# Optimization experiments

Measured on AMD Instinct MI355X. Metric: run time of the kernel, lower is better.

## Reference

```python
import jax, jax.numpy as jnp
import numpy as np

P, NL, NQ, L, P2L, P2Q, D = 50000, 2000, 6000, 8, 128, 64, 32
MAX_MODELS, NPOL, MAXQ, ITERS = 7, 4, 3, 8
ZS = {'traffic': (1385.4059, 859.8119), 'packets': (1.4015, 0.8933), 'eq_lambda': (1350.9712, 858.3162), 'avg_pkts_lambda': (0.9117, 0.9724), 'exp_max_factor': (6.6636, 4.7151), 'pkts_lambda_on': (0.9116, 1.6513), 'avg_t_off': (1.6649, 2.3564), 'avg_t_on': (1.6649, 2.3564), 'ar_a': (0.0, 1.0), 'sigma': (0.0, 1.0), 'capacity': (27611.0918, 20090.6211), 'queue_size': (30259.1055, 21410.0957)}


def _glorot(k, fin, fout):
    lim = float(np.sqrt(6.0 / (fin + fout)))
    return jax.random.uniform(k, (fin, fout), jnp.float32, -lim, lim)


def setup_inputs():
    keys = iter(jax.random.split(jax.random.key(0), 80))
    nk = lambda: next(keys)
    u = lambda shape, lo=0.0, hi=1.0: jax.random.uniform(nk(), shape, jnp.float32, lo, hi)
    inp = {}
    inp['traffic'] = u((P, 1), 1.0, 3000.0)
    inp['packets'] = u((P, 1), 0.5, 3.0)
    inp['eq_lambda'] = u((P, 1), 1.0, 3000.0)
    inp['avg_pkts_lambda'] = u((P, 1))
    inp['exp_max_factor'] = u((P, 1), 1.0, 12.0)
    inp['pkts_lambda_on'] = u((P, 1))
    inp['avg_t_off'] = u((P, 1), 0.1, 4.0)
    inp['avg_t_on'] = u((P, 1), 0.1, 4.0)
    inp['ar_a'] = jax.random.normal(nk(), (P, 1), jnp.float32)
    inp['sigma'] = jax.random.normal(nk(), (P, 1), jnp.float32)
    inp['capacity'] = u((NL, 1), 8000.0, 60000.0)
    inp['queue_size'] = u((NQ, 1), 1000.0, 64000.0)
    inp['weight'] = u((NQ, 1))
    length = jax.random.randint(nk(), (P,), 1, L + 1)
    inp['length'] = length
    inp['model'] = jax.random.randint(nk(), (P,), 0, MAX_MODELS)
    inp['policy'] = jax.random.randint(nk(), (NL,), 0, NPOL)
    inp['priority'] = jax.random.randint(nk(), (NQ,), 0, MAXQ)
    inp['queue_to_path'] = jax.random.randint(nk(), (P, L), 0, NQ)
    inp['link_to_path'] = jax.random.randint(nk(), (P, L), 0, NL)
    p2l_path = jax.random.randint(nk(), (NL, P2L), 0, P)
    inp['path_to_link'] = jnp.stack([p2l_path, jnp.zeros_like(p2l_path)], -1)
    inp['p2l_deg'] = jax.random.randint(nk(), (NL,), 1, P2L + 1)
    pq_path = jax.random.randint(nk(), (NQ, P2Q), 0, P)
    pq_pos = 1 + jax.random.randint(nk(), (NQ, P2Q), 0, L) % length[pq_path]
    inp['path_to_queue'] = jnp.stack([pq_path, pq_pos], -1)
    inp['p2q_deg'] = jax.random.randint(nk(), (NQ,), 1, P2Q + 1)
    inp['queue_to_link'] = jnp.arange(NL * MAXQ).reshape(NL, MAXQ)
    def dense(fin, fout):
        return _glorot(nk(), fin, fout), jnp.zeros((fout,), jnp.float32)
    inp['pe_w1'], inp['pe_b1'] = dense(10 + MAX_MODELS, D)
    inp['pe_w2'], inp['pe_b2'] = dense(D, D)
    inp['le_w1'], inp['le_b1'] = dense(NPOL + 1, D)
    inp['le_w2'], inp['le_b2'] = dense(D, D)
    inp['qe_w1'], inp['qe_b1'] = dense(MAXQ + 2, D)
    inp['qe_w2'], inp['qe_b2'] = dense(D, D)
    inp['prW'] = _glorot(nk(), 2 * D, D); inp['prU'] = _glorot(nk(), D, D); inp['prB'] = jnp.zeros((D,), jnp.float32)
    inp['qrW'] = _glorot(nk(), D, D); inp['qrU'] = _glorot(nk(), D, D); inp['qrB'] = jnp.zeros((D,), jnp.float32)
    inp['lrW'] = _glorot(nk(), D, D); inp['lrU'] = _glorot(nk(), D, D); inp['lrB'] = jnp.zeros((D,), jnp.float32)
    inp['ro_w1'], inp['ro_b1'] = dense(D, D // 2)
    inp['ro_w2'], inp['ro_b2'] = dense(D // 2, D // 2)
    inp['ro_w3'], inp['ro_b3'] = dense(D // 2, 1)
    return inp


def _mlp2(x, w1, b1, w2, b2):
    return jax.nn.relu(jax.nn.relu(x @ w1 + b1) @ w2 + b2)


def _forward(traffic, packets, eq_lambda, avg_pkts_lambda, exp_max_factor, pkts_lambda_on,
             avg_t_off, avg_t_on, ar_a, sigma, capacity, queue_size, weight,
             pe_w1, pe_b1, pe_w2, pe_b2, le_w1, le_b1, le_w2, le_b2, qe_w1, qe_b1, qe_w2, qe_b2,
             prW, prU, prB, qrW, qrU, qrB, lrW, lrU, lrB,
             ro_w1, ro_b1, ro_w2, ro_b2, ro_w3, ro_b3,
             length, model, policy, priority, queue_to_path, link_to_path,
             path_to_link, path_to_queue, queue_to_link, p2l_deg, p2q_deg):
    dt = traffic.dtype
    nz = lambda x, k: (x - ZS[k][0]) / ZS[k][1]
    # link load: masked ragged sum of traffic of paths crossing each link
    p2l_mask = (jnp.arange(P2L) < p2l_deg[:, None]).astype(dt)                # [NL, P2L]
    path_gather_traffic = traffic[path_to_link[:, :, 0], 0]                   # [NL, P2L]
    load = (path_gather_traffic * p2l_mask).sum(1, keepdims=True) / capacity  # [NL, 1]
    pkt_size = traffic / packets                                              # [P, 1]
    path_features = jnp.concatenate([
        nz(traffic, 'traffic'), nz(packets, 'packets'),
        jax.nn.one_hot(model, MAX_MODELS, dtype=dt),
        nz(eq_lambda, 'eq_lambda'), nz(avg_pkts_lambda, 'avg_pkts_lambda'),
        nz(exp_max_factor, 'exp_max_factor'), nz(pkts_lambda_on, 'pkts_lambda_on'),
        nz(avg_t_off, 'avg_t_off'), nz(avg_t_on, 'avg_t_on'),
        nz(ar_a, 'ar_a'), nz(sigma, 'sigma')], axis=1)                         # [P, 17]
    path_state = _mlp2(path_features, pe_w1, pe_b1, pe_w2, pe_b2)             # [P, D]
    link_state = _mlp2(jnp.concatenate([load, jax.nn.one_hot(policy, NPOL, dtype=dt)], 1),
                       le_w1, le_b1, le_w2, le_b2)                             # [NL, D]
    queue_state = _mlp2(jnp.concatenate([nz(queue_size, 'queue_size'),
                                         jax.nn.one_hot(priority, MAXQ, dtype=dt), weight], 1),
                        qe_w1, qe_b1, qe_w2, qe_b2)                            # [NQ, D]
    hop_mask = (jnp.arange(L) < length[:, None]).astype(dt)                    # [P, L]
    p2q_mask = (jnp.arange(P2Q) < p2q_deg[:, None]).astype(dt)                 # [NQ, P2Q]

    def path_step(h, xs):
        x_t, m_t = xs
        h_new = jnp.tanh(x_t @ prW + h @ prU + prB)
        h = m_t[:, None] * h_new + (1.0 - m_t[:, None]) * h  # ragged: freeze past length
        return h, h

    pss = None
    for _ in range(ITERS):
        qg = queue_state[queue_to_path]                                        # [P, L, D]
        lg = link_state[link_to_path]                                          # [P, L, D]
        xin = jnp.concatenate([qg, lg], -1)                                    # [P, L, 2D]
        prev = path_state
        path_state, seq = jax.lax.scan(path_step, path_state,
                                       (jnp.swapaxes(xin, 0, 1), hop_mask.T))
        pss = jnp.concatenate([prev[:, None], jnp.swapaxes(seq, 0, 1)], 1)     # [P, L+1, D]
        pg = pss[path_to_queue[:, :, 0], path_to_queue[:, :, 1]]               # [NQ, P2Q, D]
        path_sum = (pg * p2q_mask[:, :, None]).sum(1)                          # [NQ, D]
        queue_state = jnp.tanh(path_sum @ qrW + queue_state @ qrU + qrB)
        qgl = queue_state[queue_to_link]                                       # [NL, 3, D]
        h = link_state
        for t in range(MAXQ):  # fixed tiny sequence of 3 queues per link
            h = jnp.tanh(qgl[:, t] @ lrW + h @ lrU + lrB)
        link_state = h
    cap_g = capacity[link_to_path, 0]                                          # [P, L]
    occ = jax.nn.relu(pss[:, 1:] @ ro_w1 + ro_b1)
    occ = jax.nn.relu(occ @ ro_w2 + ro_b2)
    occ = (occ @ ro_w3 + ro_b3)[:, :, 0]                                       # [P, L]
    queue_delay = ((occ / cap_g) * hop_mask).sum(1, keepdims=True)             # [P, 1]
    trans_delay = pkt_size * ((1.0 / cap_g) * hop_mask).sum(1, keepdims=True)  # [P, 1]
    return queue_delay + trans_delay


def reference(traffic, packets, eq_lambda, avg_pkts_lambda, exp_max_factor, pkts_lambda_on,
              avg_t_off, avg_t_on, ar_a, sigma, capacity, queue_size, weight,
              pe_w1, pe_b1, pe_w2, pe_b2, le_w1, le_b1, le_w2, le_b2, qe_w1, qe_b1, qe_w2, qe_b2,
              prW, prU, prB, qrW, qrU, qrB, lrW, lrU, lrB,
              ro_w1, ro_b1, ro_w2, ro_b2, ro_w3, ro_b3,
              length, model, policy, priority, queue_to_path, link_to_path,
              path_to_link, path_to_queue, queue_to_link, p2l_deg, p2q_deg):
    return _forward(traffic, packets, eq_lambda, avg_pkts_lambda, exp_max_factor, pkts_lambda_on,
                    avg_t_off, avg_t_on, ar_a, sigma, capacity, queue_size, weight,
                    pe_w1, pe_b1, pe_w2, pe_b2, le_w1, le_b1, le_w2, le_b2, qe_w1, qe_b1, qe_w2, qe_b2,
                    prW, prU, prB, qrW, qrU, qrB, lrW, lrU, lrB,
                    ro_w1, ro_b1, ro_w2, ro_b2, ro_w3, ro_b3,
                    length, model, policy, priority, queue_to_path, link_to_path,
                    path_to_link, path_to_queue, queue_to_link, p2l_deg, p2q_deg)
```

## Files before the change

kernel.cpp:

```cpp
#include <hip/hip_runtime.h>
#include <hip/hip_bf16.h>

#define P_ 50000
#define NL_ 2000
#define NQ_ 6000
#define L_ 8
#define P2L_ 128
#define P2Q_ 64
#define D_ 32
#define ITERS_ 8
#define RA_ 1563
#define RC_ 1500

typedef __hip_bfloat16 bf16;
typedef unsigned short u16;
typedef unsigned int u32;

__device__ __forceinline__ float bfb2f(u16 u) {
    union { u32 i; float f; } c; c.i = ((u32)u) << 16; return c.f;
}
__device__ __forceinline__ u16 f2bfb(float f) {
    union { bf16 h; u16 u; } c; c.h = __float2bfloat16(f); return c.u;
}
__device__ __forceinline__ u32 pk2(float a, float b) {
    return (u32)f2bfb(a) | ((u32)f2bfb(b) << 16);
}

__device__ __forceinline__ float tanh_fast(float x) {
    return 1.f - 2.f / (__expf(2.f * x) + 1.f);
}
__device__ __forceinline__ float4 tanh4(float4 a) {
    return make_float4(tanh_fast(a.x), tanh_fast(a.y), tanh_fast(a.z), tanh_fast(a.w));
}

__device__ __forceinline__ void hr_rebuild(float* hr, float4 own) {
    hr[0] = own.x; hr[1] = own.y; hr[2] = own.z; hr[3] = own.w;
#pragma unroll
    for (int c = 0; c < 4; c++)  hr[4 + c]  = __shfl_xor(hr[c], 1, 64);
#pragma unroll
    for (int c = 0; c < 8; c++)  hr[8 + c]  = __shfl_xor(hr[c], 2, 64);
#pragma unroll
    for (int c = 0; c < 16; c++) hr[16 + c] = __shfl_xor(hr[c], 4, 64);
}

__device__ __forceinline__ float4 matvec32o(const float* hr, const float* base,
                                            const int* offs, float4 acc) {
#pragma unroll
    for (int s = 0; s < 8; s++) {
        const float* u0 = base + offs[s];
#pragma unroll
        for (int c = 0; c < 4; c++) {
            const float4 u = *(const float4*)(u0 + 32 * c);
            const float hk = hr[4 * s + c];
            acc.x += hk * u.x; acc.y += hk * u.y;
            acc.z += hk * u.z; acc.w += hk * u.w;
        }
    }
    return acc;
}

__device__ bool detect_f32(const void* p, int n) {
    const u16* u = (const u16*)p;
    int m = n < 64 ? n : 64;
    bool bad = false;
    for (int k = 0; k < m; k++) {
        float v = bfb2f(u[k]);
        float av = fabsf(v);
        bool sane = (v == v) && (av <= 1e6f) && (av == 0.0f || av >= 1e-8f);
        bad |= !sane;
    }
    return bad;
}


struct CvtArgs { const void* p[40]; };

__global__ __launch_bounds__(256) void k_convert(CvtArgs a, float* __restrict__ dst,
                                                 int* __restrict__ counters) {
    static constexpr int N[40] = {
        50000,50000,50000,50000,50000,50000,50000,50000,50000,50000,
        2000,6000,6000,
        544,32,1024,32, 160,32,1024,32, 160,32,1024,32,
        2048,1024,32, 1024,1024,32, 1024,1024,32,
        512,16,256,16,16,1};
    if (blockIdx.x == 0 && threadIdx.x < 16) counters[threadIdx.x] = 0;
    int b = blockIdx.x, t = 0, off = 0;
    for (;;) {
        int nb = (N[t] + 255) >> 8;
        if (b < nb) break;
        b -= nb; off += N[t]; ++t;
    }
    const void* src = a.p[t];
    const int n = N[t];
    const bool isf = detect_f32(src, n);
    if (t == 0 && b == 0 && threadIdx.x == 0) counters[16] = isf ? 1 : 0;
    const int i = b * 256 + threadIdx.x;
    if (i < n)
        dst[off + i] = isf ? ((const float*)src)[i] : bfb2f(((const u16*)src)[i]);
}


__global__ __launch_bounds__(256) void k_hist(const int* __restrict__ length,
                                              int* __restrict__ hist) {
    __shared__ int hc[8];
    const int tid = threadIdx.x;
    if (tid < 8) hc[tid] = 0;
    __syncthreads();
    int p = blockIdx.x * 256 + tid;
    if (p < P_) atomicAdd(&hc[length[p] - 1], 1);
    __syncthreads();
    if (tid < 8 && hc[tid] > 0) atomicAdd(&hist[tid], hc[tid]);
}

__global__ __launch_bounds__(256) void k_scatter(const int* __restrict__ length,
                                                 const int* __restrict__ hist,
                                                 int* __restrict__ cursor,
                                                 int* __restrict__ perm,
                                                 int* __restrict__ inv) {
    __shared__ int cnt[8];
    __shared__ int base[8];
    const int tid = threadIdx.x;
    if (tid < 8) cnt[tid] = 0;
    __syncthreads();
    const int p = blockIdx.x * 256 + tid;
    int b = 0, r = 0;
    if (p < P_) { b = length[p] - 1; r = atomicAdd(&cnt[b], 1); }
    __syncthreads();
    if (tid < 8) {
        int pre = 0;
#pragma unroll
        for (int k = 0; k < 8; k++) pre += (k > tid) ? hist[k] : 0;
        base[tid] = pre + (cnt[tid] > 0 ? atomicAdd(&cursor[tid], cnt[tid]) : 0);
    }
    __syncthreads();
    if (p < P_) { const int pos = base[b] + r; perm[pos] = p; inv[p] = pos; }
}


__global__ __launch_bounds__(256) void k_remap(
    const int* __restrict__ perm, const int* __restrict__ inv,
    const int* __restrict__ q2p, const int* __restrict__ l2p,
    const int* __restrict__ length, const int* __restrict__ p2q,
    int* __restrict__ q2ps, int* __restrict__ l2ps, int* __restrict__ lens,
    int* __restrict__ p2qs)
{
    const int blk = blockIdx.x;
    if (blk < RA_) {
        const int idx = blk * 256 + threadIdx.x;
        if (idx >= P_ * 8) return;
        const int j = idx >> 3, t = idx & 7;
        const int p = perm[j];
        q2ps[idx] = q2p[p * 8 + t];
        l2ps[idx] = l2p[p * 8 + t];
        if (t == 0) lens[j] = length[p];
    } else {
        const int e = (blk - RA_) * 256 + threadIdx.x;
        if (e >= NQ_ * P2Q_) return;
        const int2 pr = ((const int2*)p2q)[e];
        ((int2*)p2qs)[e] = make_int2(inv[pr.x], pr.y);
    }
}


__global__ __launch_bounds__(256) void k_path_embed(
    const float* __restrict__ traffic, const float* __restrict__ packets,
    const float* __restrict__ eq_lambda, const float* __restrict__ avg_pkts_lambda,
    const float* __restrict__ exp_max_factor, const float* __restrict__ pkts_lambda_on,
    const float* __restrict__ avg_t_off, const float* __restrict__ avg_t_on,
    const float* __restrict__ ar_a, const float* __restrict__ sigma,
    const int* __restrict__ model, const int* __restrict__ inv,
    const float* __restrict__ w1, const float* __restrict__ b1,
    const float* __restrict__ w2, const float* __restrict__ b2,
    float* __restrict__ sps)
{
    __shared__ float s_w1[544], s_w2[1024], s_b1[32], s_b2[32];
    const int tid = threadIdx.x;
    for (int idx = tid; idx < 544; idx += 256)  s_w1[idx] = w1[idx];
    for (int idx = tid; idx < 1024; idx += 256) s_w2[idx] = w2[idx];
    if (tid < 32) { s_b1[tid] = b1[tid]; s_b2[tid] = b2[tid]; }
    __syncthreads();

    int p = blockIdx.x * 256 + tid;
    if (p >= P_) return;
    float f[10];
    f[0] = (traffic[p]        - 1385.4059f) * (1.f / 859.8119f);
    f[1] = (packets[p]        - 1.4015f)    * (1.f / 0.8933f);
    f[2] = (eq_lambda[p]      - 1350.9712f) * (1.f / 858.3162f);
    f[3] = (avg_pkts_lambda[p]- 0.9117f)    * (1.f / 0.9724f);
    f[4] = (exp_max_factor[p] - 6.6636f)    * (1.f / 4.7151f);
    f[5] = (pkts_lambda_on[p] - 0.9116f)    * (1.f / 1.6513f);
    f[6] = (avg_t_off[p]      - 1.6649f)    * (1.f / 2.3564f);
    f[7] = (avg_t_on[p]       - 1.6649f)    * (1.f / 2.3564f);
    f[8] = ar_a[p];
    f[9] = sigma[p];
    const int mrow = 2 + model[p];
    float h1[32];
#pragma unroll
    for (int d = 0; d < 32; d++) {
        float a = s_b1[d] + s_w1[mrow * 32 + d];
        a += f[0] * s_w1[0 * 32 + d];
        a += f[1] * s_w1[1 * 32 + d];
#pragma unroll
        for (int j = 0; j < 8; j++) a += f[2 + j] * s_w1[(9 + j) * 32 + d];
        h1[d] = fmaxf(a, 0.f);
    }
    float* dst = sps + (size_t)inv[p] * 32;
#pragma unroll
    for (int d = 0; d < 32; d++) {
        float a = s_b2[d];
#pragma unroll
        for (int k = 0; k < 32; k++) a += h1[k] * s_w2[k * 32 + d];
        dst[d] = fmaxf(a, 0.f);
    }
}


__global__ __launch_bounds__(256) void k_queue_embed(
    const float* __restrict__ queue_size, const float* __restrict__ weight,
    const int* __restrict__ priority,
    const float* __restrict__ w1, const float* __restrict__ b1,
    const float* __restrict__ w2, const float* __restrict__ b2,
    const float* __restrict__ prW, const float* __restrict__ prB,
    float* __restrict__ queue_state, float* __restrict__ zq)
{
    __shared__ float s_w1[160], s_w2[1024], s_pw[1024], s_b1[32], s_b2[32], s_pb[32];
    const int tid = threadIdx.x;
    if (tid < 160) s_w1[tid] = w1[tid];
    for (int idx = tid; idx < 1024; idx += 256) {
        s_w2[idx] = w2[idx];
        s_pw[idx] = prW[idx];
    }
    if (tid < 32) { s_b1[tid] = b1[tid]; s_b2[tid] = b2[tid]; s_pb[tid] = prB[tid]; }
    __syncthreads();

    int q = blockIdx.x * 256 + tid;
    if (q >= NQ_) return;
    float f0 = (queue_size[q] - 30259.1055f) * (1.f / 21410.0957f);
    float f4 = weight[q];
    int prow = 1 + priority[q];
    float h1[32];
#pragma unroll
    for (int d = 0; d < 32; d++) {
        float a = s_b1[d] + s_w1[prow * 32 + d]
                + f0 * s_w1[0 * 32 + d] + f4 * s_w1[4 * 32 + d];
        h1[d] = fmaxf(a, 0.f);
    }
    float h2[32];
#pragma unroll
    for (int d = 0; d < 32; d++) {
        float a = s_b2[d];
#pragma unroll
        for (int k = 0; k < 32; k++) a += h1[k] * s_w2[k * 32 + d];
        h2[d] = fmaxf(a, 0.f);
        queue_state[q * 32 + d] = h2[d];
    }
#pragma unroll
    for (int d = 0; d < 32; d++) {
        float a = s_pb[d];
#pragma unroll
        for (int k = 0; k < 32; k++) a += h2[k] * s_pw[k * 32 + d];
        zq[q * 32 + d] = a;
    }
}


__global__ __launch_bounds__(256) void k_link_embed(
    const float* __restrict__ traffic, const float* __restrict__ capacity,
    const int* __restrict__ policy,
    const int* __restrict__ p2l, const int* __restrict__ p2l_deg,
    const float* __restrict__ w1, const float* __restrict__ b1,
    const float* __restrict__ w2, const float* __restrict__ b2,
    const float* __restrict__ prWl,
    float* __restrict__ link_state, float* __restrict__ zl)
{
    __shared__ float wsh[2272];
    __shared__ float h1s[4][32];
    __shared__ float h2s[4][32];
    const int tid = threadIdx.x;
    if (tid < 160) wsh[tid] = w1[tid];
    if (tid < 32)  wsh[160 + tid] = b1[tid];
    for (int idx = tid; idx < 1024; idx += 256) {
        wsh[192 + idx]  = w2[idx];
        wsh[1248 + idx] = prWl[idx];
    }
    if (tid >= 32 && tid < 64) wsh[1216 + tid - 32] = b2[tid - 32];
    __syncthreads();

    const int w = tid >> 6, lane = tid & 63;
    const int l = blockIdx.x * 4 + w;
    const int deg = p2l_deg[l];
    float s = 0.f;
    if (lane < deg)      s += traffic[p2l[l * 256 + 2 * lane]];
    if (lane + 64 < deg) s += traffic[p2l[l * 256 + 2 * (lane + 64)]];
#pragma unroll
    for (int m = 1; m < 64; m <<= 1) s += __shfl_xor(s, m, 64);
    const float load = s / capacity[l];
    const int prow = 1 + policy[l];
    if (lane < 32) {
        float a = wsh[160 + lane] + wsh[prow * 32 + lane] + load * wsh[lane];
        h1s[w][lane] = fmaxf(a, 0.f);
    }
    __syncthreads();
    if (lane < 32) {
        float a = wsh[1216 + lane];
#pragma unroll
        for (int k = 0; k < 32; k++) a += h1s[w][k] * wsh[192 + k * 32 + lane];
        a = fmaxf(a, 0.f);
        link_state[l * 32 + lane] = a;
        h2s[w][lane] = a;
    }
    __syncthreads();
    if (lane < 32) {
        float a = 0.f;
#pragma unroll
        for (int k = 0; k < 32; k++) a += h2s[w][k] * wsh[1248 + k * 32 + lane];
        zl[l * 32 + lane] = a;
    }
}


__global__ __launch_bounds__(256, 2) void k_path_rnn(
    const int* __restrict__ q2ps, const int* __restrict__ l2ps,
    const int* __restrict__ lens,
    const float* __restrict__ prU,
    const float* __restrict__ zq, const float* __restrict__ zl,
    float* __restrict__ sps, u16* __restrict__ pss)
{
    const int tid = threadIdx.x;
    const int grp = tid >> 3, i = tid & 7;
    const int j = blockIdx.x * 32 + grp;
    if (j >= P_) return;
    const int len = lens[j];

    float4 Ub[32];
#pragma unroll
    for (int s = 0; s < 8; s++) {
        const float* rb = prU + ((i ^ s) * 128 + 4 * i);
#pragma unroll
        for (int c = 0; c < 4; c++)
            Ub[4 * s + c] = *(const float4*)(rb + 32 * c);
    }

    const int4 qi0 = *(const int4*)(q2ps + (size_t)j * 8);
    const int4 qi1 = *(const int4*)(q2ps + (size_t)j * 8 + 4);
    const int4 li0 = *(const int4*)(l2ps + (size_t)j * 8);
    const int4 li1 = *(const int4*)(l2ps + (size_t)j * 8 + 4);
    const int qidx[8] = {qi0.x, qi0.y, qi0.z, qi0.w, qi1.x, qi1.y, qi1.z, qi1.w};
    const int lidx[8] = {li0.x, li0.y, li0.z, li0.w, li1.x, li1.y, li1.z, li1.w};

    float4 own = *(const float4*)(sps + (size_t)j * 32 + 4 * i);
    float hr[32];
    hr_rebuild(hr, own);

    float4 z;
    {
        const float4 a = *(const float4*)(zq + (size_t)qidx[0] * 32 + 4 * i);
        const float4 b = *(const float4*)(zl + (size_t)lidx[0] * 32 + 4 * i);
        z = make_float4(a.x + b.x, a.y + b.y, a.z + b.z, a.w + b.w);
    }

#pragma unroll
    for (int t = 0; t < 8; t++) {
        if (t >= len) break;
        float4 acc = z;
        if (t + 1 < len) {
            const float4 a = *(const float4*)(zq + (size_t)qidx[t + 1] * 32 + 4 * i);
            const float4 b = *(const float4*)(zl + (size_t)lidx[t + 1] * 32 + 4 * i);
            z = make_float4(a.x + b.x, a.y + b.y, a.z + b.z, a.w + b.w);
        }
#pragma unroll
        for (int k = 0; k < 32; k++) {
            const float hk = hr[k];
            acc.x += hk * Ub[k].x; acc.y += hk * Ub[k].y;
            acc.z += hk * Ub[k].z; acc.w += hk * Ub[k].w;
        }
        own = tanh4(acc);
        uint2 w2;
        w2.x = pk2(own.x, own.y);
        w2.y = pk2(own.z, own.w);
        *(uint2*)(pss + (size_t)j * 256 + t * 32 + 4 * i) = w2;
        if (t + 1 < len) hr_rebuild(hr, own);
    }
    *(float4*)(sps + (size_t)j * 32 + 4 * i) = own;
}


__global__ __launch_bounds__(256, 2) void k_rnn_last(
    const int* __restrict__ q2ps, const int* __restrict__ l2ps,
    const int* __restrict__ lens, const int* __restrict__ perm,
    const float* __restrict__ prU,
    const float* __restrict__ zq, const float* __restrict__ zl,
    const float* __restrict__ sps,
    const float* __restrict__ capacity,
    const float* __restrict__ traffic, const float* __restrict__ packets,
    const float* __restrict__ w1, const float* __restrict__ b1,
    const float* __restrict__ w2, const float* __restrict__ b2,
    const float* __restrict__ w3, const float* __restrict__ b3,
    const int* __restrict__ flags, void* __restrict__ out)
{
    __shared__ float wl[817];
    const int tid = threadIdx.x;
    for (int idx = tid; idx < 512; idx += 256) wl[idx] = w1[idx];
    if (tid < 256) wl[528 + tid] = w2[tid];
    if (tid < 16) {
        wl[512 + tid] = b1[tid];
        wl[784 + tid] = b2[tid];
        wl[800 + tid] = w3[tid];
    }
    if (tid == 0) wl[816] = b3[0];
    __syncthreads();

    const int grp = tid >> 3, i = tid & 7;
    const int j = blockIdx.x * 32 + grp;
    if (j >= P_) return;
    const int len = lens[j];

    float4 Ub[32];
#pragma unroll
    for (int s = 0; s < 8; s++) {
        const float* rb = prU + ((i ^ s) * 128 + 4 * i);
#pragma unroll
        for (int c = 0; c < 4; c++)
            Ub[4 * s + c] = *(const float4*)(rb + 32 * c);
    }

    const int4 qi0 = *(const int4*)(q2ps + (size_t)j * 8);
    const int4 qi1 = *(const int4*)(q2ps + (size_t)j * 8 + 4);
    const int4 li0 = *(const int4*)(l2ps + (size_t)j * 8);
    const int4 li1 = *(const int4*)(l2ps + (size_t)j * 8 + 4);
    const int qidx[8] = {qi0.x, qi0.y, qi0.z, qi0.w, qi1.x, qi1.y, qi1.z, qi1.w};
    const int lidx[8] = {li0.x, li0.y, li0.z, li0.w, li1.x, li1.y, li1.z, li1.w};

    float4 own = *(const float4*)(sps + (size_t)j * 32 + 4 * i);
    float hr[32];
    hr_rebuild(hr, own);

    float4 z;
    {
        const float4 a = *(const float4*)(zq + (size_t)qidx[0] * 32 + 4 * i);
        const float4 b = *(const float4*)(zl + (size_t)lidx[0] * 32 + 4 * i);
        z = make_float4(a.x + b.x, a.y + b.y, a.z + b.z, a.w + b.w);
    }

    float qd = 0.f, ts = 0.f;
#pragma unroll
    for (int t = 0; t < 8; t++) {
        if (t >= len) break;
        float4 acc = z;
        if (t + 1 < len) {
            const float4 a = *(const float4*)(zq + (size_t)qidx[t + 1] * 32 + 4 * i);
            const float4 b = *(const float4*)(zl + (size_t)lidx[t + 1] * 32 + 4 * i);
            z = make_float4(a.x + b.x, a.y + b.y, a.z + b.z, a.w + b.w);
        }
#pragma unroll
        for (int k = 0; k < 32; k++) {
            const float hk = hr[k];
            acc.x += hk * Ub[k].x; acc.y += hk * Ub[k].y;
            acc.z += hk * Ub[k].z; acc.w += hk * Ub[k].w;
        }
        own = tanh4(acc);
        hr_rebuild(hr, own);

        float a0 = wl[512 + 2 * i], a1 = wl[512 + 2 * i + 1];
#pragma unroll
        for (int s = 0; s < 8; s++) {
#pragma unroll
            for (int c = 0; c < 4; c++) {
                const int k = 4 * (i ^ s) + c;
                const float2 u = *(const float2*)&wl[k * 16 + 2 * i];
                const float hk = hr[4 * s + c];
                a0 += hk * u.x; a1 += hk * u.y;
            }
        }
        a0 = fmaxf(a0, 0.f); a1 = fmaxf(a1, 0.f);
        float h2r[16];
        h2r[0] = a0; h2r[1] = a1;
#pragma unroll
        for (int c = 0; c < 2; c++) h2r[2 + c] = __shfl_xor(h2r[c], 1, 64);
#pragma unroll
        for (int c = 0; c < 4; c++) h2r[4 + c] = __shfl_xor(h2r[c], 2, 64);
#pragma unroll
        for (int c = 0; c < 8; c++) h2r[8 + c] = __shfl_xor(h2r[c], 4, 64);
        float c0 = wl[784 + 2 * i], c1 = wl[784 + 2 * i + 1];
#pragma unroll
        for (int s = 0; s < 8; s++) {
#pragma unroll
            for (int c = 0; c < 2; c++) {
                const int k = 2 * (i ^ s) + c;
                const float2 u = *(const float2*)&wl[528 + k * 16 + 2 * i];
                const float hk = h2r[2 * s + c];
                c0 += hk * u.x; c1 += hk * u.y;
            }
        }
        c0 = fmaxf(c0, 0.f); c1 = fmaxf(c1, 0.f);
        float pv = c0 * wl[800 + 2 * i] + c1 * wl[800 + 2 * i + 1];
        pv += __shfl_xor(pv, 1, 8);
        pv += __shfl_xor(pv, 2, 8);
        pv += __shfl_xor(pv, 4, 8);
        const float occv = pv + wl[816];
        const float inv = 1.f / capacity[lidx[t]];
        qd += occv * inv;
        ts += inv;
    }
    if (i == 0) {
        const int p = perm[j];
        const float res = qd + (traffic[p] / packets[p]) * ts;
        if (flags[0]) ((float*)out)[p] = res;
        else          ((bf16*)out)[p] = __float2bfloat16(res);
    }
}


__global__ __launch_bounds__(256) void k_queue_update(
    const int* __restrict__ p2qs, const int* __restrict__ p2q_deg,
    const float* __restrict__ qrW, const float* __restrict__ qrU,
    const float* __restrict__ qrB,
    const float* __restrict__ prWq, const float* __restrict__ prB,
    const u16* __restrict__ pss, float* __restrict__ queue_state,
    float* __restrict__ zq)
{
    __shared__ float wl[3 * 1024 + 64];
    const int tid = threadIdx.x;
#pragma unroll
    for (int jj = 0; jj < 4; jj++) {
        wl[tid + 256 * jj]        = qrW[tid + 256 * jj];
        wl[1024 + tid + 256 * jj] = qrU[tid + 256 * jj];
        wl[2048 + tid + 256 * jj] = prWq[tid + 256 * jj];
    }
    if (tid < 32) { wl[3072 + tid] = qrB[tid]; wl[3104 + tid] = prB[tid]; }
    __syncthreads();

    const int w = tid >> 6, lane = tid & 63;
    const int g = lane >> 3, i = lane & 7;
    const int q = blockIdx.x * 4 + w;
    const int deg = p2q_deg[q];

    int offs[8];
#pragma unroll
    for (int s = 0; s < 8; s++) offs[s] = (i ^ s) * 128 + 4 * i;

    float4 ps = {0.f, 0.f, 0.f, 0.f};
    for (int j = g; j < deg; j += 8) {
        const int2 pr = ((const int2*)p2qs)[q * 64 + j];
        int pos = pr.y - 1;
        pos = pos < 0 ? 0 : (pos > 7 ? 7 : pos);
        const ushort4 v = *(const ushort4*)(pss + (size_t)pr.x * 256 + pos * 32 + 4 * i);
        ps.x += bfb2f(v.x); ps.y += bfb2f(v.y);
        ps.z += bfb2f(v.z); ps.w += bfb2f(v.w);
    }
#pragma unroll
    for (int m = 8; m < 64; m <<= 1) {
        ps.x += __shfl_xor(ps.x, m, 64);
        ps.y += __shfl_xor(ps.y, m, 64);
        ps.z += __shfl_xor(ps.z, m, 64);
        ps.w += __shfl_xor(ps.w, m, 64);
    }
    const float4 qs = *(const float4*)(queue_state + (size_t)q * 32 + 4 * i);

    float psr[32]; hr_rebuild(psr, ps);
    float qsr[32]; hr_rebuild(qsr, qs);
    float4 acc = *(const float4*)(wl + 3072 + 4 * i);
    acc = matvec32o(psr, wl, offs, acc);
    acc = matvec32o(qsr, wl + 1024, offs, acc);
    const float4 nh = tanh4(acc);

    float nhr[32]; hr_rebuild(nhr, nh);
    float4 zacc = *(const float4*)(wl + 3104 + 4 * i);
    zacc = matvec32o(nhr, wl + 2048, offs, zacc);

    if (g == 0) {
        *(float4*)(queue_state + (size_t)q * 32 + 4 * i) = nh;
        *(float4*)(zq + (size_t)q * 32 + 4 * i) = zacc;
    }
}


__global__ __launch_bounds__(256) void k_link_update(
    const int* __restrict__ q2l,
    const float* __restrict__ lrW, const float* __restrict__ lrU,
    const float* __restrict__ lrB,
    const float* __restrict__ prWl,
    const float* __restrict__ queue_state, float* __restrict__ link_state,
    float* __restrict__ zl)
{
    __shared__ float wl[3 * 1024 + 32];
    const int tid = threadIdx.x;
#pragma unroll
    for (int jj = 0; jj < 4; jj++) {
        wl[tid + 256 * jj]        = lrW[tid + 256 * jj];
        wl[1024 + tid + 256 * jj] = lrU[tid + 256 * jj];
        wl[2048 + tid + 256 * jj] = prWl[tid + 256 * jj];
    }
    if (tid < 32) wl[3072 + tid] = lrB[tid];
    __syncthreads();

    const int w = tid >> 6, lane = tid & 63;
    const int i = lane & 7, g = lane >> 3;
    const int l = blockIdx.x * 4 + w;

    int offs[8];
#pragma unroll
    for (int s = 0; s < 8; s++) offs[s] = (i ^ s) * 128 + 4 * i;

    float4 h = *(const float4*)(link_state + (size_t)l * 32 + 4 * i);
    float hhr[32]; hr_rebuild(hhr, h);

#pragma unroll
    for (int t = 0; t < 3; t++) {
        const int qq = q2l[l * 3 + t];
        const float4 qg = *(const float4*)(queue_state + (size_t)qq * 32 + 4 * i);
        float qgr[32]; hr_rebuild(qgr, qg);
        float4 acc = *(const float4*)(wl + 3072 + 4 * i);
        acc = matvec32o(qgr, wl, offs, acc);
        acc = matvec32o(hhr, wl + 1024, offs, acc);
        h = tanh4(acc);
        hr_rebuild(hhr, h);
    }
    float4 zacc = make_float4(0.f, 0.f, 0.f, 0.f);
    zacc = matvec32o(hhr, wl + 2048, offs, zacc);
    if (g == 0) {
        *(float4*)(link_state + (size_t)l * 32 + 4 * i) = h;
        *(float4*)(zl + (size_t)l * 32 + 4 * i) = zacc;
    }
}


extern "C" void kernel_launch(void* const* d_in, const int* in_sizes, int n_in,
                              void* d_out, int out_size, void* d_ws, size_t ws_size,
                              hipStream_t stream)
{
    static const int CVT_N[40] = {
        50000,50000,50000,50000,50000,50000,50000,50000,50000,50000,
        2000,6000,6000,
        544,32,1024,32, 160,32,1024,32, 160,32,1024,32,
        2048,1024,32, 1024,1024,32, 1024,1024,32,
        512,16,256,16,16,1};

    const int*  length   = (const int*)d_in[13];
    const int*  model    = (const int*)d_in[14];
    const int*  policy   = (const int*)d_in[15];
    const int*  priority = (const int*)d_in[16];
    const int*  q2p      = (const int*)d_in[17];
    const int*  l2p      = (const int*)d_in[18];
    const int*  p2l      = (const int*)d_in[19];
    const int*  p2l_deg  = (const int*)d_in[20];
    const int*  p2q      = (const int*)d_in[21];
    const int*  p2q_deg  = (const int*)d_in[22];
    const int*  q2l      = (const int*)d_in[23];

    CvtArgs ca;
    for (int i = 0; i < 13; i++) ca.p[i] = d_in[i];
    for (int i = 0; i < 27; i++) ca.p[13 + i] = d_in[24 + i];

    int off[41]; off[0] = 0;
    for (int i = 0; i < 40; i++) off[i + 1] = off[i] + CVT_N[i];
    int nblk = 0;
    for (int i = 0; i < 40; i++) nblk += (CVT_N[i] + 255) / 256;

    float* ws = (float*)d_ws;
    const float* c_traffic    = ws + off[0];
    const float* c_packets    = ws + off[1];
    const float* c_eq_lambda  = ws + off[2];
    const float* c_apl        = ws + off[3];
    const float* c_emf        = ws + off[4];
    const float* c_plo        = ws + off[5];
    const float* c_atoff      = ws + off[6];
    const float* c_aton       = ws + off[7];
    const float* c_ar_a       = ws + off[8];
    const float* c_sigma      = ws + off[9];
    const float* c_capacity   = ws + off[10];
    const float* c_queue_size = ws + off[11];
    const float* c_weight     = ws + off[12];
    const float* c_pe_w1 = ws + off[13]; const float* c_pe_b1 = ws + off[14];
    const float* c_pe_w2 = ws + off[15]; const float* c_pe_b2 = ws + off[16];
    const float* c_le_w1 = ws + off[17]; const float* c_le_b1 = ws + off[18];
    const float* c_le_w2 = ws + off[19]; const float* c_le_b2 = ws + off[20];
    const float* c_qe_w1 = ws + off[21]; const float* c_qe_b1 = ws + off[22];
    const float* c_qe_w2 = ws + off[23]; const float* c_qe_b2 = ws + off[24];
    const float* c_prW = ws + off[25]; const float* c_prU = ws + off[26];
    const float* c_prB = ws + off[27];
    const float* c_qrW = ws + off[28]; const float* c_qrU = ws + off[29];
    const float* c_qrB = ws + off[30];
    const float* c_lrW = ws + off[31]; const float* c_lrU = ws + off[32];
    const float* c_lrB = ws + off[33];
    const float* c_ro_w1 = ws + off[34]; const float* c_ro_b1 = ws + off[35];
    const float* c_ro_w2 = ws + off[36]; const float* c_ro_b2 = ws + off[37];
    const float* c_ro_w3 = ws + off[38]; const float* c_ro_b3 = ws + off[39];

    size_t base = ((size_t)off[40] + 63) & ~(size_t)63;
    float* sps         = ws + base;
    float* queue_state = sps + (size_t)P_ * 32;
    float* link_state  = queue_state + (size_t)NQ_ * 32;
    float* zq          = link_state + (size_t)NL_ * 32;
    float* zl          = zq + (size_t)NQ_ * 32;
    u16*   pss         = (u16*)(zl + (size_t)NL_ * 32);
    int*   perm        = (int*)(pss + (size_t)P_ * 256);
    int*   inv         = perm + P_;
    int*   lens        = inv + P_;
    int*   q2ps        = lens + P_;
    int*   l2ps        = q2ps + (size_t)P_ * 8;
    int*   p2qs        = l2ps + (size_t)P_ * 8;
    int*   counters    = p2qs + (size_t)NQ_ * 2 * P2Q_;
    int*   hist        = counters;
    int*   cursor      = counters + 8;
    int*   flags       = counters + 16;

    k_convert<<<nblk, 256, 0, stream>>>(ca, ws, counters);
    k_hist<<<(P_ + 255) / 256, 256, 0, stream>>>(length, hist);
    k_scatter<<<(P_ + 255) / 256, 256, 0, stream>>>(length, hist, cursor, perm, inv);
    k_remap<<<RA_ + RC_, 256, 0, stream>>>(
        perm, inv, q2p, l2p, length, p2q, q2ps, l2ps, lens, p2qs);

    k_path_embed<<<(P_ + 255) / 256, 256, 0, stream>>>(
        c_traffic, c_packets, c_eq_lambda, c_apl, c_emf, c_plo, c_atoff, c_aton,
        c_ar_a, c_sigma, model, inv, c_pe_w1, c_pe_b1, c_pe_w2, c_pe_b2, sps);
    k_queue_embed<<<(NQ_ + 255) / 256, 256, 0, stream>>>(
        c_queue_size, c_weight, priority, c_qe_w1, c_qe_b1, c_qe_w2, c_qe_b2,
        c_prW, c_prB, queue_state, zq);
    k_link_embed<<<NL_ / 4, 256, 0, stream>>>(
        c_traffic, c_capacity, policy, p2l, p2l_deg,
        c_le_w1, c_le_b1, c_le_w2, c_le_b2, c_prW + 1024, link_state, zl);

    for (int it = 0; it < ITERS_ - 1; ++it) {
        k_path_rnn<<<(P_ + 31) / 32, 256, 0, stream>>>(
            q2ps, l2ps, lens, c_prU, zq, zl, sps, pss);
        k_queue_update<<<NQ_ / 4, 256, 0, stream>>>(
            p2qs, p2q_deg, c_qrW, c_qrU, c_qrB, c_prW, c_prB,
            pss, queue_state, zq);
        k_link_update<<<NL_ / 4, 256, 0, stream>>>(
            q2l, c_lrW, c_lrU, c_lrB, c_prW + 1024,
            queue_state, link_state, zl);
    }

    k_rnn_last<<<(P_ + 31) / 32, 256, 0, stream>>>(
        q2ps, l2ps, lens, perm, c_prU, zq, zl, sps,
        c_capacity, c_traffic, c_packets,
        c_ro_w1, c_ro_b1, c_ro_w2, c_ro_b2, c_ro_w3, c_ro_b3,
        flags, d_out);
}
```

Before: 642.5 us.

## Fuse queue and link updates into one kernel and split matvec accumulators

Merges the per-iteration queue update and link update into one 512-thread kernel. Six waves update the three queues feeding each of two links, stage the new queue states in shared memory, and after a block barrier two waves run the link GRU-style recurrence from those shared states. This removes one launch per iteration and the global round trip of queue_state between kernels, but it assumes every queue belongs to exactly one link through q2l. Matvecs in all kernels now use two independent accumulators for more instruction-level parallelism. The path RNN kernels' launch bounds are relaxed to one block per CU minimum, which may raise register use and reduce occupancy.

After: 1.591 ms. 2.48x slower.

```diff
diff --git a/kernel.cpp b/kernel.cpp
--- a/kernel.cpp
+++ b/kernel.cpp
@@ -32,6 +32,9 @@
 __device__ __forceinline__ float4 tanh4(float4 a) {
     return make_float4(tanh_fast(a.x), tanh_fast(a.y), tanh_fast(a.z), tanh_fast(a.w));
 }
+__device__ __forceinline__ float4 add4(float4 a, float4 b) {
+    return make_float4(a.x + b.x, a.y + b.y, a.z + b.z, a.w + b.w);
+}
 
 __device__ __forceinline__ void hr_rebuild(float* hr, float4 own) {
     hr[0] = own.x; hr[1] = own.y; hr[2] = own.z; hr[3] = own.w;
@@ -45,18 +48,24 @@
 
 __device__ __forceinline__ float4 matvec32o(const float* hr, const float* base,
                                             const int* offs, float4 acc) {
-#pragma unroll
-    for (int s = 0; s < 8; s++) {
+    float4 acc2 = make_float4(0.f, 0.f, 0.f, 0.f);
+#pragma unroll
+    for (int s = 0; s < 4; s++) {
         const float* u0 = base + offs[s];
+        const float* u1 = base + offs[s + 4];
 #pragma unroll
         for (int c = 0; c < 4; c++) {
             const float4 u = *(const float4*)(u0 + 32 * c);
             const float hk = hr[4 * s + c];
             acc.x += hk * u.x; acc.y += hk * u.y;
             acc.z += hk * u.z; acc.w += hk * u.w;
-        }
-    }
-    return acc;
+            const float4 v = *(const float4*)(u1 + 32 * c);
+            const float hk2 = hr[4 * (s + 4) + c];
+            acc2.x += hk2 * v.x; acc2.y += hk2 * v.y;
+            acc2.z += hk2 * v.z; acc2.w += hk2 * v.w;
+        }
+    }
+    return add4(acc, acc2);
 }
 
 __device__ bool detect_f32(const void* p, int n) {
@@ -319,7 +328,7 @@
 }
 
 
-__global__ __launch_bounds__(256, 2) void k_path_rnn(
+__global__ __launch_bounds__(256, 1) void k_path_rnn(
     const int* __restrict__ q2ps, const int* __restrict__ l2ps,
     const int* __restrict__ lens,
     const float* __restrict__ prU,
@@ -356,25 +365,29 @@
     {
         const float4 a = *(const float4*)(zq + (size_t)qidx[0] * 32 + 4 * i);
         const float4 b = *(const float4*)(zl + (size_t)lidx[0] * 32 + 4 * i);
-        z = make_float4(a.x + b.x, a.y + b.y, a.z + b.z, a.w + b.w);
+        z = add4(a, b);
     }
 
 #pragma unroll
     for (int t = 0; t < 8; t++) {
         if (t >= len) break;
-        float4 acc = z;
+        float4 accA = z;
+        float4 accB = make_float4(0.f, 0.f, 0.f, 0.f);
         if (t + 1 < len) {
             const float4 a = *(const float4*)(zq + (size_t)qidx[t + 1] * 32 + 4 * i);
             const float4 b = *(const float4*)(zl + (size_t)lidx[t + 1] * 32 + 4 * i);
-            z = make_float4(a.x + b.x, a.y + b.y, a.z + b.z, a.w + b.w);
-        }
-#pragma unroll
-        for (int k = 0; k < 32; k++) {
+            z = add4(a, b);
+        }
+#pragma unroll
+        for (int k = 0; k < 16; k++) {
             const float hk = hr[k];
-            acc.x += hk * Ub[k].x; acc.y += hk * Ub[k].y;
-            acc.z += hk * Ub[k].z; acc.w += hk * Ub[k].w;
-        }
-        own = tanh4(acc);
+            accA.x += hk * Ub[k].x; accA.y += hk * Ub[k].y;
+            accA.z += hk * Ub[k].z; accA.w += hk * Ub[k].w;
+            const float hk2 = hr[k + 16];
+            accB.x += hk2 * Ub[k + 16].x; accB.y += hk2 * Ub[k + 16].y;
+            accB.z += hk2 * Ub[k + 16].z; accB.w += hk2 * Ub[k + 16].w;
+        }
+        own = tanh4(add4(accA, accB));
         uint2 w2;
         w2.x = pk2(own.x, own.y);
         w2.y = pk2(own.z, own.w);
@@ -385,7 +398,7 @@
 }
 
 
-__global__ __launch_bounds__(256, 2) void k_rnn_last(
+__global__ __launch_bounds__(256, 1) void k_rnn_last(
     const int* __restrict__ q2ps, const int* __restrict__ l2ps,
     const int* __restrict__ lens, const int* __restrict__ perm,
     const float* __restrict__ prU,
@@ -439,40 +452,49 @@
     {
         const float4 a = *(const float4*)(zq + (size_t)qidx[0] * 32 + 4 * i);
         const float4 b = *(const float4*)(zl + (size_t)lidx[0] * 32 + 4 * i);
-        z = make_float4(a.x + b.x, a.y + b.y, a.z + b.z, a.w + b.w);
+        z = add4(a, b);
     }
 
     float qd = 0.f, ts = 0.f;
 #pragma unroll
     for (int t = 0; t < 8; t++) {
         if (t >= len) break;
-        float4 acc = z;
+        float4 accA = z;
+        float4 accB = make_float4(0.f, 0.f, 0.f, 0.f);
         if (t + 1 < len) {
             const float4 a = *(const float4*)(zq + (size_t)qidx[t + 1] * 32 + 4 * i);
             const float4 b = *(const float4*)(zl + (size_t)lidx[t + 1] * 32 + 4 * i);
-            z = make_float4(a.x + b.x, a.y + b.y, a.z + b.z, a.w + b.w);
-        }
-#pragma unroll
-        for (int k = 0; k < 32; k++) {
+            z = add4(a, b);
+        }
+#pragma unroll
+        for (int k = 0; k < 16; k++) {
             const float hk = hr[k];
-            acc.x += hk * Ub[k].x; acc.y += hk * Ub[k].y;
-            acc.z += hk * Ub[k].z; acc.w += hk * Ub[k].w;
-        }
-        own = tanh4(acc);
+            accA.x += hk * Ub[k].x; accA.y += hk * Ub[k].y;
+            accA.z += hk * Ub[k].z; accA.w += hk * Ub[k].w;
+            const float hk2 = hr[k + 16];
+            accB.x += hk2 * Ub[k + 16].x; accB.y += hk2 * Ub[k + 16].y;
+            accB.z += hk2 * Ub[k + 16].z; accB.w += hk2 * Ub[k + 16].w;
+        }
+        own = tanh4(add4(accA, accB));
         hr_rebuild(hr, own);
 
         float a0 = wl[512 + 2 * i], a1 = wl[512 + 2 * i + 1];
-#pragma unroll
-        for (int s = 0; s < 8; s++) {
+        float b0 = 0.f, b1v = 0.f;
+#pragma unroll
+        for (int s = 0; s < 4; s++) {
 #pragma unroll
             for (int c = 0; c < 4; c++) {
                 const int k = 4 * (i ^ s) + c;
                 const float2 u = *(const float2*)&wl[k * 16 + 2 * i];
                 const float hk = hr[4 * s + c];
                 a0 += hk * u.x; a1 += hk * u.y;
+                const int k2 = 4 * (i ^ (s + 4)) + c;
+                const float2 u2 = *(const float2*)&wl[k2 * 16 + 2 * i];
+                const float hk2 = hr[4 * (s + 4) + c];
+                b0 += hk2 * u2.x; b1v += hk2 * u2.y;
             }
         }
-        a0 = fmaxf(a0, 0.f); a1 = fmaxf(a1, 0.f);
+        a0 = fmaxf(a0 + b0, 0.f); a1 = fmaxf(a1 + b1v, 0.f);
         float h2r[16];
         h2r[0] = a0; h2r[1] = a1;
 #pragma unroll
@@ -482,17 +504,22 @@
 #pragma unroll
         for (int c = 0; c < 8; c++) h2r[8 + c] = __shfl_xor(h2r[c], 4, 64);
         float c0 = wl[784 + 2 * i], c1 = wl[784 + 2 * i + 1];
-#pragma unroll
-        for (int s = 0; s < 8; s++) {
+        float d0 = 0.f, d1 = 0.f;
+#pragma unroll
+        for (int s = 0; s < 4; s++) {
 #pragma unroll
             for (int c = 0; c < 2; c++) {
                 const int k = 2 * (i ^ s) + c;
                 const float2 u = *(const float2*)&wl[528 + k * 16 + 2 * i];
                 const float hk = h2r[2 * s + c];
                 c0 += hk * u.x; c1 += hk * u.y;
+                const int k2 = 2 * (i ^ (s + 4)) + c;
+                const float2 u2 = *(const float2*)&wl[528 + k2 * 16 + 2 * i];
+                const float hk2 = h2r[2 * (s + 4) + c];
+                d0 += hk2 * u2.x; d1 += hk2 * u2.y;
             }
         }
-        c0 = fmaxf(c0, 0.f); c1 = fmaxf(c1, 0.f);
+        c0 = fmaxf(c0 + d0, 0.f); c1 = fmaxf(c1 + d1, 0.f);
         float pv = c0 * wl[800 + 2 * i] + c1 * wl[800 + 2 * i + 1];
         pv += __shfl_xor(pv, 1, 8);
         pv += __shfl_xor(pv, 2, 8);
@@ -511,116 +538,99 @@
 }
 
 
-__global__ __launch_bounds__(256) void k_queue_update(
+__global__ __launch_bounds__(512) void k_qlupd(
     const int* __restrict__ p2qs, const int* __restrict__ p2q_deg,
+    const int* __restrict__ q2l,
     const float* __restrict__ qrW, const float* __restrict__ qrU,
     const float* __restrict__ qrB,
-    const float* __restrict__ prWq, const float* __restrict__ prB,
-    const u16* __restrict__ pss, float* __restrict__ queue_state,
-    float* __restrict__ zq)
-{
-    __shared__ float wl[3 * 1024 + 64];
-    const int tid = threadIdx.x;
-#pragma unroll
-    for (int jj = 0; jj < 4; jj++) {
-        wl[tid + 256 * jj]        = qrW[tid + 256 * jj];
-        wl[1024 + tid + 256 * jj] = qrU[tid + 256 * jj];
-        wl[2048 + tid + 256 * jj] = prWq[tid + 256 * jj];
-    }
-    if (tid < 32) { wl[3072 + tid] = qrB[tid]; wl[3104 + tid] = prB[tid]; }
-    __syncthreads();
-
-    const int w = tid >> 6, lane = tid & 63;
-    const int g = lane >> 3, i = lane & 7;
-    const int q = blockIdx.x * 4 + w;
-    const int deg = p2q_deg[q];
-
-    int offs[8];
-#pragma unroll
-    for (int s = 0; s < 8; s++) offs[s] = (i ^ s) * 128 + 4 * i;
-
-    float4 ps = {0.f, 0.f, 0.f, 0.f};
-    for (int j = g; j < deg; j += 8) {
-        const int2 pr = ((const int2*)p2qs)[q * 64 + j];
-        int pos = pr.y - 1;
-        pos = pos < 0 ? 0 : (pos > 7 ? 7 : pos);
-        const ushort4 v = *(const ushort4*)(pss + (size_t)pr.x * 256 + pos * 32 + 4 * i);
-        ps.x += bfb2f(v.x); ps.y += bfb2f(v.y);
-        ps.z += bfb2f(v.z); ps.w += bfb2f(v.w);
-    }
-#pragma unroll
-    for (int m = 8; m < 64; m <<= 1) {
-        ps.x += __shfl_xor(ps.x, m, 64);
-        ps.y += __shfl_xor(ps.y, m, 64);
-        ps.z += __shfl_xor(ps.z, m, 64);
-        ps.w += __shfl_xor(ps.w, m, 64);
-    }
-    const float4 qs = *(const float4*)(queue_state + (size_t)q * 32 + 4 * i);
-
-    float psr[32]; hr_rebuild(psr, ps);
-    float qsr[32]; hr_rebuild(qsr, qs);
-    float4 acc = *(const float4*)(wl + 3072 + 4 * i);
-    acc = matvec32o(psr, wl, offs, acc);
-    acc = matvec32o(qsr, wl + 1024, offs, acc);
-    const float4 nh = tanh4(acc);
-
-    float nhr[32]; hr_rebuild(nhr, nh);
-    float4 zacc = *(const float4*)(wl + 3104 + 4 * i);
-    zacc = matvec32o(nhr, wl + 2048, offs, zacc);
-
-    if (g == 0) {
-        *(float4*)(queue_state + (size_t)q * 32 + 4 * i) = nh;
-        *(float4*)(zq + (size_t)q * 32 + 4 * i) = zacc;
-    }
-}
-
-
-__global__ __launch_bounds__(256) void k_link_update(
-    const int* __restrict__ q2l,
     const float* __restrict__ lrW, const float* __restrict__ lrU,
     const float* __restrict__ lrB,
-    const float* __restrict__ prWl,
-    const float* __restrict__ queue_state, float* __restrict__ link_state,
-    float* __restrict__ zl)
+    const float* __restrict__ prW, const float* __restrict__ prB,
+    const u16* __restrict__ pss, float* __restrict__ queue_state,
+    float* __restrict__ link_state,
+    float* __restrict__ zq, float* __restrict__ zl)
 {
-    __shared__ float wl[3 * 1024 + 32];
+    __shared__ float wl[6 * 1024 + 96 + 192];
     const int tid = threadIdx.x;
-#pragma unroll
-    for (int jj = 0; jj < 4; jj++) {
-        wl[tid + 256 * jj]        = lrW[tid + 256 * jj];
-        wl[1024 + tid + 256 * jj] = lrU[tid + 256 * jj];
-        wl[2048 + tid + 256 * jj] = prWl[tid + 256 * jj];
-    }
-    if (tid < 32) wl[3072 + tid] = lrB[tid];
-    __syncthreads();
-
-    const int w = tid >> 6, lane = tid & 63;
-    const int i = lane & 7, g = lane >> 3;
-    const int l = blockIdx.x * 4 + w;
-
+    for (int idx = tid; idx < 1024; idx += 512) {
+        wl[idx]        = qrW[idx];
+        wl[1024 + idx] = qrU[idx];
+        wl[2048 + idx] = prW[idx];
+        wl[3072 + idx] = lrW[idx];
+        wl[4096 + idx] = lrU[idx];
+        wl[5120 + idx] = prW[1024 + idx];
+    }
+    if (tid < 32) {
+        wl[6144 + tid] = qrB[tid];
+        wl[6176 + tid] = prB[tid];
+        wl[6208 + tid] = lrB[tid];
+    }
+    __syncthreads();
+
+    const int wv = tid >> 6, lane = tid & 63;
+    const int g = lane >> 3, i = lane & 7;
     int offs[8];
 #pragma unroll
     for (int s = 0; s < 8; s++) offs[s] = (i ^ s) * 128 + 4 * i;
-
-    float4 h = *(const float4*)(link_state + (size_t)l * 32 + 4 * i);
-    float hhr[32]; hr_rebuild(hhr, h);
-
-#pragma unroll
-    for (int t = 0; t < 3; t++) {
-        const int qq = q2l[l * 3 + t];
-        const float4 qg = *(const float4*)(queue_state + (size_t)qq * 32 + 4 * i);
-        float qgr[32]; hr_rebuild(qgr, qg);
-        float4 acc = *(const float4*)(wl + 3072 + 4 * i);
-        acc = matvec32o(qgr, wl, offs, acc);
-        acc = matvec32o(hhr, wl + 1024, offs, acc);
-        h = tanh4(acc);
-        hr_rebuild(hhr, h);
-    }
-    float4 zacc = make_float4(0.f, 0.f, 0.f, 0.f);
-    zacc = matvec32o(hhr, wl + 2048, offs, zacc);
-    if (g == 0) {
-        *(float4*)(link_state + (size_t)l * 32 + 4 * i) = h;
-        *(float4*)(zl + (size_t)l * 32 + 4 * i) = zacc;
+    float* qsh = wl + 6240;
+
+    if (wv < 6) {
+        const int l = blockIdx.x * 2 + (wv / 3);
+        const int q = q2l[l * 3 + (wv % 3)];
+        const int deg = p2q_deg[q];
+        float4 ps = {0.f, 0.f, 0.f, 0.f};
+        for (int j = g; j < deg; j += 8) {
+            const int2 pr = ((const int2*)p2qs)[q * 64 + j];
+            int pos = pr.y - 1;
+            pos = pos < 0 ? 0 : (pos > 7 ? 7 : pos);
+            const ushort4 v = *(const ushort4*)(pss + (size_t)pr.x * 256 + pos * 32 + 4 * i);
+            ps.x += bfb2f(v.x); ps.y += bfb2f(v.y);
+            ps.z += bfb2f(v.z); ps.w += bfb2f(v.w);
+        }
+#pragma unroll
+        for (int m = 8; m < 64; m <<= 1) {
+            ps.x += __shfl_xor(ps.x, m, 64);
+            ps.y += __shfl_xor(ps.y, m, 64);
+            ps.z += __shfl_xor(ps.z, m, 64);
+            ps.w += __shfl_xor(ps.w, m, 64);
+        }
+        const float4 qs = *(const float4*)(queue_state + (size_t)q * 32 + 4 * i);
+        float psr[32]; hr_rebuild(psr, ps);
+        float qsr[32]; hr_rebuild(qsr, qs);
+        float4 accA = *(const float4*)(wl + 6144 + 4 * i);
+        accA = matvec32o(psr, wl, offs, accA);
+        float4 accB = matvec32o(qsr, wl + 1024, offs, make_float4(0.f, 0.f, 0.f, 0.f));
+        const float4 nh = tanh4(add4(accA, accB));
+        float nhr[32]; hr_rebuild(nhr, nh);
+        float4 zacc = *(const float4*)(wl + 6176 + 4 * i);
+        zacc = matvec32o(nhr, wl + 2048, offs, zacc);
+        if (g == 0) {
+            *(float4*)(queue_state + (size_t)q * 32 + 4 * i) = nh;
+            *(float4*)(zq + (size_t)q * 32 + 4 * i) = zacc;
+            *(float4*)(qsh + wv * 32 + 4 * i) = nh;
+        }
+    }
+    __syncthreads();
+    if (wv >= 6) {
+        const int li = wv - 6;
+        const int l = blockIdx.x * 2 + li;
+        float4 h = *(const float4*)(link_state + (size_t)l * 32 + 4 * i);
+        float hhr[32]; hr_rebuild(hhr, h);
+#pragma unroll
+        for (int c = 0; c < 3; c++) {
+            const float4 qg = *(const float4*)(qsh + (li * 3 + c) * 32 + 4 * i);
+            float qgr[32]; hr_rebuild(qgr, qg);
+            float4 accA = *(const float4*)(wl + 6208 + 4 * i);
+            accA = matvec32o(qgr, wl + 3072, offs, accA);
+            float4 accB = matvec32o(hhr, wl + 4096, offs, make_float4(0.f, 0.f, 0.f, 0.f));
+            h = tanh4(add4(accA, accB));
+            hr_rebuild(hhr, h);
+        }
+        float4 zacc = matvec32o(hhr, wl + 5120, offs, make_float4(0.f, 0.f, 0.f, 0.f));
+        if (g == 0) {
+            *(float4*)(link_state + (size_t)l * 32 + 4 * i) = h;
+            *(float4*)(zl + (size_t)l * 32 + 4 * i) = zacc;
+        }
     }
 }
 
@@ -724,12 +734,9 @@
     for (int it = 0; it < ITERS_ - 1; ++it) {
         k_path_rnn<<<(P_ + 31) / 32, 256, 0, stream>>>(
             q2ps, l2ps, lens, c_prU, zq, zl, sps, pss);
-        k_queue_update<<<NQ_ / 4, 256, 0, stream>>>(
-            p2qs, p2q_deg, c_qrW, c_qrU, c_qrB, c_prW, c_prB,
-            pss, queue_state, zq);
-        k_link_update<<<NL_ / 4, 256, 0, stream>>>(
-            q2l, c_lrW, c_lrU, c_lrB, c_prW + 1024,
-            queue_state, link_state, zl);
+        k_qlupd<<<NL_ / 2, 512, 0, stream>>>(
+            p2qs, p2q_deg, q2l, c_qrW, c_qrU, c_qrB, c_lrW, c_lrU, c_lrB,
+            c_prW, c_prB, pss, queue_state, link_state, zq, zl);
     }
 
     k_rnn_last<<<(P_ + 31) / 32, 256, 0, stream>>>(
```
